# Performance work log

Hardware: AMD Instinct MI355X
Metric: run time of the kernel (lower is better)

## Reference

```python
import jax, jax.numpy as jnp
import numpy as np

B, S, D, H = 256, 512, 128, 256  # batch, seq_len, input_dim, hidden_dim


def setup_inputs() -> dict:
    key = jax.random.key(0)
    ks = jax.random.split(key, 7)
    scale = 1.0 / np.sqrt(H)
    return {
        "x": jax.random.normal(ks[0], (B, S, D), dtype=jnp.float32),
        # WU_e: Linear(2H + S -> S, bias=False)
        "W_ue": jax.random.uniform(ks[1], (S, 2 * H + S), dtype=jnp.float32, minval=-scale, maxval=scale),
        # v_e: Linear(S -> 1, bias=False)
        "v_e": jax.random.uniform(ks[2], (1, S), dtype=jnp.float32, minval=-scale, maxval=scale),
        # LSTM params (PyTorch layout: gates order i,f,g,o)
        "W_ih": jax.random.uniform(ks[3], (4 * H, D), dtype=jnp.float32, minval=-scale, maxval=scale),
        "W_hh": jax.random.uniform(ks[4], (4 * H, H), dtype=jnp.float32, minval=-scale, maxval=scale),
        "b_ih": jax.random.uniform(ks[5], (4 * H,), dtype=jnp.float32, minval=-scale, maxval=scale),
        "b_hh": jax.random.uniform(ks[6], (4 * H,), dtype=jnp.float32, minval=-scale, maxval=scale),
    }


def reference(x, W_ue, v_e, W_ih, W_hh, b_ih, b_hh):
    b = x.shape[0]
    hdim = W_hh.shape[1]
    # Split WU_e into the part acting on (h,c) and the part acting on x rows.
    W_h = W_ue[:, : 2 * hdim]          # [S, 2H]
    W_x = W_ue[:, 2 * hdim:]           # [S, S]
    xT = jnp.transpose(x, (0, 2, 1))   # [B, D, S]
    # x contribution to attention logits is the same every step -> precompute.
    proj_x = jnp.einsum("bds,os->bdo", xT, W_x)  # [B, D, S]
    v = v_e[0]                          # [S]
    xs = jnp.transpose(x, (1, 0, 2))    # [S, B, D]

    def step(carry, x_t):
        h, c = carry                                    # [B, H] each
        hs = jnp.concatenate([h, c], axis=-1)           # [B, 2H]
        proj_h = hs @ W_h.T                             # [B, S]
        t = jnp.tanh(proj_h[:, None, :] + proj_x)       # [B, D, S]
        E = jnp.einsum("bds,s->bd", t, v)               # [B, D]
        alpha = jax.nn.softmax(E, axis=1)               # [B, D]
        inp = x_t * alpha                               # [B, D]
        gates = inp @ W_ih.T + b_ih + h @ W_hh.T + b_hh # [B, 4H]
        i, f, g, o = jnp.split(gates, 4, axis=-1)
        i = jax.nn.sigmoid(i)
        f = jax.nn.sigmoid(f)
        g = jnp.tanh(g)
        o = jax.nn.sigmoid(o)
        c_new = f * c + i * g
        h_new = o * jnp.tanh(c_new)
        return (h_new, c_new), h_new

    h0 = jnp.zeros((b, hdim), dtype=x.dtype)
    c0 = jnp.zeros((b, hdim), dtype=x.dtype)
    _, x_encoded = jax.lax.scan(step, (h0, c0), xs)  # [S, B, H]
    return x_encoded
```

## Files before the change

### kernel.cpp

```cpp
#include <hip/hip_runtime.h>
#include <hip/hip_bf16.h>

typedef __attribute__((ext_vector_type(8))) short bf16x8;
typedef __attribute__((ext_vector_type(4))) float f32x4;

#define C2LE 2.8853900817779268f
#define LOG2E 1.4426950408889634f
#define AGENT __HIP_MEMORY_SCOPE_AGENT
#define RLX __ATOMIC_RELAXED

static __device__ __forceinline__ float blo(unsigned q) { return __uint_as_float(q << 16); }
static __device__ __forceinline__ float bhi(unsigned q) { return __uint_as_float(q & 0xFFFF0000u); }
static __device__ __forceinline__ float sigm(float x) {
  return __builtin_amdgcn_rcpf(1.0f + __builtin_amdgcn_exp2f(-x * LOG2E));
}
static __device__ __forceinline__ float tanhe(float x) {
  return fmaf(-2.0f, __builtin_amdgcn_rcpf(1.0f + __builtin_amdgcn_exp2f(x * C2LE)), 1.0f);
}
static __device__ __forceinline__ unsigned packhilo(float x) {
  __hip_bfloat16 h = __float2bfloat16(x);
  float r = x - __bfloat162float(h);
  __hip_bfloat16 l = __float2bfloat16(r);
  return (unsigned)__bfloat16_as_ushort(h) | ((unsigned)__bfloat16_as_ushort(l) << 16);
}
static __device__ __forceinline__ void mkfrags(uint4 q0, uint4 q1, bf16x8& hi, bf16x8& lo) {
  uint4 h, l;
  h.x = __builtin_amdgcn_perm(q0.y, q0.x, 0x05040100u);
  h.y = __builtin_amdgcn_perm(q0.w, q0.z, 0x05040100u);
  h.z = __builtin_amdgcn_perm(q1.y, q1.x, 0x05040100u);
  h.w = __builtin_amdgcn_perm(q1.w, q1.z, 0x05040100u);
  l.x = __builtin_amdgcn_perm(q0.y, q0.x, 0x07060302u);
  l.y = __builtin_amdgcn_perm(q0.w, q0.z, 0x07060302u);
  l.z = __builtin_amdgcn_perm(q1.y, q1.x, 0x07060302u);
  l.w = __builtin_amdgcn_perm(q1.w, q1.z, 0x07060302u);
  hi = *(bf16x8*)&h;
  lo = *(bf16x8*)&l;
}
static __device__ __forceinline__ int swz(int e) { return e ^ ((e >> 4) & 7); }

__global__ void k_pack_whB(const float* __restrict__ wue, __hip_bfloat16* __restrict__ wp) {
  for (int idx = blockIdx.x * blockDim.x + threadIdx.x; idx < 262144;
       idx += gridDim.x * blockDim.x) {
    int j = idx & 7, l = (idx >> 3) & 63, kap = (idx >> 9) & 15, nb = (idx >> 13) & 3,
        sl = idx >> 15;
    int o = sl * 64 + nb * 16 + (l & 15);
    int dim = kap * 32 + (l >> 4) * 8 + j;
    wp[idx] = __float2bfloat16(wue[o * 1024 + dim]);
  }
}
__global__ void k_pack_w3B(const float* __restrict__ wih, const float* __restrict__ whh,
                           __hip_bfloat16* __restrict__ wp) {
  for (int idx = blockIdx.x * blockDim.x + threadIdx.x; idx < 393216;
       idx += gridDim.x * blockDim.x) {
    int j = idx & 7, l = (idx >> 3) & 63;
    int ks = (idx >> 9) % 12, r = (idx >> 9) / 12;
    int nb = r & 7, sl = r >> 3;
    int n = nb * 16 + (l & 15);
    int g = (n >> 5) * 256 + sl * 32 + (n & 31);
    int k = ks * 32 + (l >> 4) * 8 + j;
    float v = (k < 128) ? wih[g * 128 + k] : whh[g * 256 + (k - 128)];
    wp[idx] = __float2bfloat16(v);
  }
}
__global__ void k_bsum(const float* __restrict__ bih, const float* __restrict__ bhh,
                       float* __restrict__ bs) {
  int idx = blockIdx.x * blockDim.x + threadIdx.x;
  if (idx < 1024) bs[idx] = bih[idx] + bhh[idx];
}
__global__ void k_wxt(const float* __restrict__ wue, float* __restrict__ wxt) {
  for (int idx = blockIdx.x * blockDim.x + threadIdx.x; idx < 512 * 512;
       idx += gridDim.x * blockDim.x) {
    int o = idx & 511, s = idx >> 9;
    wxt[idx] = wue[o * 1024 + 512 + s];
  }
}

__global__ __launch_bounds__(512) void k_projx(const float* __restrict__ x,
                                               const float* __restrict__ wxt,
                                               __hip_bfloat16* __restrict__ px2) {
  __shared__ alignas(16) float xsT[32][512];
  const int b = blockIdx.x;
  const int tid = threadIdx.x;
  for (int dt = 0; dt < 4; ++dt) {
    __syncthreads();
    const float4* xr = (const float4*)(x + ((size_t)b << 16) + (size_t)tid * 128 + dt * 32);
#pragma unroll
    for (int q = 0; q < 8; ++q) {
      float4 vx = xr[q];
      xsT[q * 4 + 0][tid] = vx.x;
      xsT[q * 4 + 1][tid] = vx.y;
      xsT[q * 4 + 2][tid] = vx.z;
      xsT[q * 4 + 3][tid] = vx.w;
    }
    __syncthreads();
    const int o = tid;
    float acc[32];
#pragma unroll
    for (int dd = 0; dd < 32; ++dd) acc[dd] = 0.f;
    for (int s4 = 0; s4 < 128; ++s4) {
      float w0 = wxt[(s4 * 4 + 0) * 512 + o];
      float w1 = wxt[(s4 * 4 + 1) * 512 + o];
      float w2 = wxt[(s4 * 4 + 2) * 512 + o];
      float w3 = wxt[(s4 * 4 + 3) * 512 + o];
#pragma unroll
      for (int dd = 0; dd < 32; ++dd) {
        float4 xv = *(const float4*)&xsT[dd][s4 * 4];
        acc[dd] = fmaf(w0, xv.x, fmaf(w1, xv.y, fmaf(w2, xv.z, fmaf(w3, xv.w, acc[dd]))));
      }
    }
    for (int dd = 0; dd < 32; ++dd) {
      px2[((size_t)b * 128 + dt * 32 + dd) * 512 + o] =
          __float2bfloat16(__builtin_amdgcn_exp2f(acc[dd] * C2LE));
    }
  }
}

__global__ __launch_bounds__(1024) void k_main(
    const __hip_bfloat16* __restrict__ px2, const __hip_bfloat16* __restrict__ whB,
    const __hip_bfloat16* __restrict__ w3B, const float* __restrict__ bsum,
    const float* __restrict__ x, const float* __restrict__ ve,
    unsigned* __restrict__ hG, float* __restrict__ Eg, unsigned* __restrict__ ctrs,
    float* __restrict__ out) {
  __shared__ alignas(16) __hip_bfloat16 w3_l[49152];
  __shared__ alignas(16) uint4 hA0[1024];
  __shared__ alignas(16) uint4 hA1[1024];
  __shared__ alignas(16) uint4 uA0[256];
  __shared__ alignas(16) uint4 uA1[256];
  __shared__ float PHp[4][8][64];
  __shared__ float PH[512];
  __shared__ float gp[2][128][9];
  __shared__ float c_l[32][8];
  __shared__ float v_l[64];
  __shared__ float bs_l[128];
  __shared__ float zpart[16];
  __shared__ float vss_sh;

  const int grp = blockIdx.x & 31;
  const int sl = blockIdx.x >> 5;
  const int tid = threadIdx.x;
  const int lane = tid & 63;
  const int w = tid >> 6;
  const int b = tid >> 7;
  const int d = tid & 127;
  const int bG = grp * 8 + b;

  {
    const uint4* src = (const uint4*)(w3B + (size_t)sl * 49152);
    uint4* dst = (uint4*)w3_l;
    for (int i = tid; i < 6144; i += 1024) dst[i] = src[i];
  }
  bf16x8 whr[4];
  {
    const bf16x8* src =
        (const bf16x8*)whB + ((size_t)(sl * 4 + (w & 3)) * 16 + (w >> 2) * 4) * 64 + lane;
#pragma unroll
    for (int i = 0; i < 4; ++i) whr[i] = src[i * 64];
  }
  uint4 pxr[8];
  {
    const uint4* p4 = (const uint4*)(px2 + ((size_t)bG * 128 + d) * 512 + sl * 64);
#pragma unroll
    for (int i = 0; i < 8; ++i) pxr[i] = p4[i];
  }
  if (tid < 64) v_l[tid] = ve[sl * 64 + tid];
  if (tid < 128) bs_l[tid] = bsum[(tid >> 5) * 256 + sl * 32 + (tid & 31)];
  if (tid < 256) c_l[tid >> 3][tid & 7] = 0.f;
  {
    uint4 z = {0, 0, 0, 0};
    hA0[tid] = z;
    hA1[tid] = z;
    if (tid < 256) {
      uA0[tid] = z;
      uA1[tid] = z;
    }
  }
  if (tid == 0) {
    float s = 0.f;
    for (int i = 0; i < 64; ++i) s += ve[sl * 64 + i];
    vss_sh = s;
  }
  __syncthreads();
  const float vss = vss_sh;
  unsigned* ctrA = ctrs + grp * 64;
  unsigned* ctrB = ctrA + 32;
  float xv = x[((size_t)bG * 512) * 128 + d];

  for (int t = 0; t < 512; ++t) {
    const int par = t & 1;

    {
      const unsigned long long* hp =
          (const unsigned long long*)(hG + (size_t)(par * 32 + grp) * 4096) + tid * 2;
      unsigned long long a0 = __hip_atomic_load(hp, RLX, AGENT);
      unsigned long long a1 = __hip_atomic_load(hp + 1, RLX, AGENT);
      int p = tid * 4;
      int e = ((p >> 6) << 4) + ((p >> 3) & 7);
      int ep = swz(e);
      uint4 q;
      q.x = (unsigned)a0;
      q.y = (unsigned)(a0 >> 32);
      q.z = (unsigned)a1;
      q.w = (unsigned)(a1 >> 32);
      if (p & 4) hA1[ep] = q;
      else hA0[ep] = q;
    }
    if (tid < 128)
      __hip_atomic_store(Eg + (size_t)((1 - par) * 32 + grp) * 1024 + sl * 128 + tid, 0.f, RLX,
                         AGENT);
    __syncthreads();

    {
      const int kq = w >> 2, nb = w & 3;
      f32x4 acc = {0.f, 0.f, 0.f, 0.f};
#pragma unroll
      for (int i = 0; i < 4; ++i) {
        int ep = swz((kq * 4 + i) * 64 + lane);
        uint4 q0 = hA0[ep], q1 = hA1[ep];
        bf16x8 ahi, alo;
        mkfrags(q0, q1, ahi, alo);
        acc = __builtin_amdgcn_mfma_f32_16x16x32_bf16(ahi, whr[i], acc, 0, 0, 0);
        acc = __builtin_amdgcn_mfma_f32_16x16x32_bf16(alo, whr[i], acc, 0, 0, 0);
      }
      if (lane < 32) {
        int r16 = lane >> 4, c16 = lane & 15;
#pragma unroll
        for (int rr = 0; rr < 4; ++rr) PHp[kq][r16 * 4 + rr][nb * 16 + c16] = acc[rr];
      }
    }
    __syncthreads();
    if (tid < 512) {
      float s = (PHp[0][tid >> 6][tid & 63] + PHp[1][tid >> 6][tid & 63] +
                 PHp[2][tid >> 6][tid & 63] + PHp[3][tid >> 6][tid & 63]);
      PH[tid] = __builtin_amdgcn_exp2f(s * C2LE);
    }
    __syncthreads();

    {
      float R = 0.f;
      const float* PHb = &PH[b * 64];
#pragma unroll 2
      for (int s8 = 0; s8 < 8; ++s8) {
        uint4 q = pxr[s8];
        float4 pa = *(const float4*)&PHb[s8 * 8];
        float4 pb = *(const float4*)&PHb[s8 * 8 + 4];
        float4 va = *(const float4*)&v_l[s8 * 8];
        float4 vb = *(const float4*)&v_l[s8 * 8 + 4];
        R = fmaf(va.x, __builtin_amdgcn_rcpf(fmaf(blo(q.x), pa.x, 1.0f)), R);
        R = fmaf(va.y, __builtin_amdgcn_rcpf(fmaf(bhi(q.x), pa.y, 1.0f)), R);
        R = fmaf(va.z, __builtin_amdgcn_rcpf(fmaf(blo(q.y), pa.z, 1.0f)), R);
        R = fmaf(va.w, __builtin_amdgcn_rcpf(fmaf(bhi(q.y), pa.w, 1.0f)), R);
        R = fmaf(vb.x, __builtin_amdgcn_rcpf(fmaf(blo(q.z), pb.x, 1.0f)), R);
        R = fmaf(vb.y, __builtin_amdgcn_rcpf(fmaf(bhi(q.z), pb.y, 1.0f)), R);
        R = fmaf(vb.z, __builtin_amdgcn_rcpf(fmaf(blo(q.w), pb.z, 1.0f)), R);
        R = fmaf(vb.w, __builtin_amdgcn_rcpf(fmaf(bhi(q.w), pb.w, 1.0f)), R);
      }
      __hip_atomic_fetch_add(Eg + (size_t)(par * 32 + grp) * 1024 + b * 128 + d,
                             fmaf(-2.f, R, vss), RLX, AGENT);
    }

    const int nb3 = w & 7, kh3 = w >> 3;
    f32x4 acc3 = {0.f, 0.f, 0.f, 0.f};
#pragma unroll
    for (int i = 0; i < 4; ++i) {
      int ks = 4 + kh3 * 4 + i;
      int ep = swz((ks - 4) * 64 + lane);
      uint4 q0 = hA0[ep], q1 = hA1[ep];
      bf16x8 ahi, alo;
      mkfrags(q0, q1, ahi, alo);
      bf16x8 bf = ((const bf16x8*)w3_l)[((size_t)nb3 * 12 + ks) * 64 + lane];
      acc3 = __builtin_amdgcn_mfma_f32_16x16x32_bf16(ahi, bf, acc3, 0, 0, 0);
      acc3 = __builtin_amdgcn_mfma_f32_16x16x32_bf16(alo, bf, acc3, 0, 0, 0);
    }
    __syncthreads();
    if (tid == 0) {
      __hip_atomic_fetch_add(ctrA, 1u, RLX, AGENT);
      while (__hip_atomic_load(ctrA, RLX, AGENT) < 8u * (t + 1)) __builtin_amdgcn_s_sleep(1);
    }
    __syncthreads();

    float Ev = __hip_atomic_load(Eg + (size_t)(par * 32 + grp) * 1024 + b * 128 + d, RLX, AGENT);
    float e = __builtin_amdgcn_exp2f(Ev * LOG2E);
    {
      float z = e;
#pragma unroll
      for (int m = 1; m < 64; m <<= 1) z += __shfl_xor(z, m);
      if (lane == 0) zpart[w] = z;
    }
    __syncthreads();
    {
      float zf = zpart[2 * b] + zpart[2 * b + 1];
      float u = xv * e * __builtin_amdgcn_rcpf(zf);
      int ep = swz((d >> 5) * 64 + ((d >> 3) & 3) * 16 + b);
      unsigned* dst = (d & 4) ? (unsigned*)&uA1[ep] : (unsigned*)&uA0[ep];
      dst[d & 3] = packhilo(u);
    }
    __syncthreads();

#pragma unroll
    for (int i = 0; i < 2; ++i) {
      int ks = kh3 * 2 + i;
      int ep = swz(ks * 64 + lane);
      uint4 q0 = uA0[ep], q1 = uA1[ep];
      bf16x8 ahi, alo;
      mkfrags(q0, q1, ahi, alo);
      bf16x8 bf = ((const bf16x8*)w3_l)[((size_t)nb3 * 12 + ks) * 64 + lane];
      acc3 = __builtin_amdgcn_mfma_f32_16x16x32_bf16(ahi, bf, acc3, 0, 0, 0);
      acc3 = __builtin_amdgcn_mfma_f32_16x16x32_bf16(alo, bf, acc3, 0, 0, 0);
    }
    if (lane < 32) {
      int r16 = lane >> 4, c16 = lane & 15;
#pragma unroll
      for (int rr = 0; rr < 4; ++rr) gp[kh3][nb3 * 16 + c16][r16 * 4 + rr] = acc3[rr];
    }
    __syncthreads();

    float h_new;
    if (tid < 256) {
      int bb = tid & 7, jj = tid >> 3;
      float gi = gp[0][jj][bb] + gp[1][jj][bb] + bs_l[jj];
      float gf = gp[0][32 + jj][bb] + gp[1][32 + jj][bb] + bs_l[32 + jj];
      float gg = gp[0][64 + jj][bb] + gp[1][64 + jj][bb] + bs_l[64 + jj];
      float go = gp[0][96 + jj][bb] + gp[1][96 + jj][bb] + bs_l[96 + jj];
      float i_ = sigm(gi), f_ = sigm(gf), g_ = tanhe(gg), o_ = sigm(go);
      float c_new = fmaf(f_, c_l[jj][bb], i_ * g_);
      h_new = o_ * tanhe(c_new);
      c_l[jj][bb] = c_new;
      int dd = sl * 32 + jj;
      int p = (((dd >> 5) * 4 + ((dd >> 3) & 3)) * 8 + bb) * 8 + (dd & 7);
      unsigned* hw = hG + (size_t)((1 - par) * 32 + grp) * 4096;
      __hip_atomic_store(hw + p, packhilo(h_new), RLX, AGENT);
      __hip_atomic_store(hw + p + 2048, packhilo(c_new), RLX, AGENT);
    }
    __syncthreads();
    if (tid == 0) __hip_atomic_fetch_add(ctrB, 1u, RLX, AGENT);
    if (tid < 256) {
      int bb = tid & 7, jj = tid >> 3;
      __builtin_nontemporal_store(h_new,
                                  out + ((size_t)t * 256 + grp * 8 + bb) * 256 + sl * 32 + jj);
    }
    int tn = (t < 511) ? t + 1 : 511;
    float xv_n = x[((size_t)bG * 512 + tn) * 128 + d];
    if (tid == 0) {
      while (__hip_atomic_load(ctrB, RLX, AGENT) < 8u * (t + 1)) __builtin_amdgcn_s_sleep(1);
    }
    __syncthreads();
    xv = xv_n;
  }
}

extern "C" void kernel_launch(void* const* d_in, const int* in_sizes, int n_in,
                              void* d_out, int out_size, void* d_ws, size_t ws_size,
                              hipStream_t stream) {
  const float* x = (const float*)d_in[0];
  const float* wue = (const float*)d_in[1];
  const float* ve = (const float*)d_in[2];
  const float* wih = (const float*)d_in[3];
  const float* whh = (const float*)d_in[4];
  const float* bih = (const float*)d_in[5];
  const float* bhh = (const float*)d_in[6];
  float* out = (float*)d_out;

  char* ws = (char*)d_ws;
  __hip_bfloat16* px2 = (__hip_bfloat16*)(ws);
  __hip_bfloat16* whB = (__hip_bfloat16*)(ws + 33554432);
  __hip_bfloat16* w3B = (__hip_bfloat16*)(ws + 34078720);
  float* bsum = (float*)(ws + 34865152);
  float* Eg = (float*)(ws + 34869248);
  unsigned* ctrs = (unsigned*)(ws + 35131392);
  unsigned* hG = (unsigned*)(ws + 35139584);
  float* wxt = (float*)(ws + 36188160);

  k_pack_whB<<<1024, 256, 0, stream>>>(wue, whB);
  k_pack_w3B<<<1024, 256, 0, stream>>>(wih, whh, w3B);
  k_bsum<<<4, 256, 0, stream>>>(bih, bhh, bsum);
  k_wxt<<<256, 256, 0, stream>>>(wue, wxt);
  k_projx<<<256, 512, 0, stream>>>(x, wxt, px2);
  hipMemsetAsync(hG, 0, 1048576, stream);
  hipMemsetAsync(Eg, 0, 262144, stream);
  hipMemsetAsync(ctrs, 0, 8192, stream);
  k_main<<<256, 1024, 0, stream>>>(px2, whB, w3B, bsum, x, ve, hG, Eg, ctrs, out);
}
```

Measured before the change: 4.631 ms.

## Replace atomic-add and counter barrier with step-tagged per-slice E partials

Each of the 8 slice blocks in a group now writes its partial attention logit as a 64-bit word tagged with the step number into its own slot, instead of atomically adding into a shared double-buffered accumulator. Consumers poll all 8 slots until every tag reaches the current step, then sum the partials locally. This removes the float atomic adds, the per-step zeroing of the other buffer, and the tid-0 counter barrier with its two __syncthreads. The cost is 8x more polling loads per thread and a larger buffer. The Eg region now overlaps wxt, which is only read by the earlier k_projx and is zeroed by a memset issued after it.

Result: slower. 8.315 ms (+79.6%).

```diff
diff --git a/kernel.cpp b/kernel.cpp
--- a/kernel.cpp
+++ b/kernel.cpp
@@ -119,8 +119,8 @@
     const __hip_bfloat16* __restrict__ px2, const __hip_bfloat16* __restrict__ whB,
     const __hip_bfloat16* __restrict__ w3B, const float* __restrict__ bsum,
     const float* __restrict__ x, const float* __restrict__ ve,
-    unsigned* __restrict__ hG, float* __restrict__ Eg, unsigned* __restrict__ ctrs,
-    float* __restrict__ out) {
+    unsigned* __restrict__ hG, unsigned long long* __restrict__ Eg,
+    unsigned* __restrict__ ctrs, float* __restrict__ out) {
   __shared__ alignas(16) __hip_bfloat16 w3_l[49152];
   __shared__ alignas(16) uint4 hA0[1024];
   __shared__ alignas(16) uint4 hA1[1024];
@@ -181,8 +181,7 @@
   }
   __syncthreads();
   const float vss = vss_sh;
-  unsigned* ctrA = ctrs + grp * 64;
-  unsigned* ctrB = ctrA + 32;
+  unsigned* ctrB = ctrs + grp * 64 + 32;
   float xv = x[((size_t)bG * 512) * 128 + d];
 
   for (int t = 0; t < 512; ++t) {
@@ -204,9 +203,6 @@
       if (p & 4) hA1[ep] = q;
       else hA0[ep] = q;
     }
-    if (tid < 128)
-      __hip_atomic_store(Eg + (size_t)((1 - par) * 32 + grp) * 1024 + sl * 128 + tid, 0.f, RLX,
-                         AGENT);
     __syncthreads();
 
     {
@@ -254,8 +250,10 @@
         R = fmaf(vb.z, __builtin_amdgcn_rcpf(fmaf(blo(q.w), pb.z, 1.0f)), R);
         R = fmaf(vb.w, __builtin_amdgcn_rcpf(fmaf(bhi(q.w), pb.w, 1.0f)), R);
       }
-      __hip_atomic_fetch_add(Eg + (size_t)(par * 32 + grp) * 1024 + b * 128 + d,
-                             fmaf(-2.f, R, vss), RLX, AGENT);
+      float part = fmaf(-2.f, R, vss);
+      unsigned long long pk =
+          ((unsigned long long)(unsigned)(t + 1) << 32) | (unsigned long long)__float_as_uint(part);
+      __hip_atomic_store(Eg + ((size_t)grp * 8 + sl) * 1024 + b * 128 + d, pk, RLX, AGENT);
     }
 
     const int nb3 = w & 7, kh3 = w >> 3;
@@ -271,15 +269,35 @@
       acc3 = __builtin_amdgcn_mfma_f32_16x16x32_bf16(ahi, bf, acc3, 0, 0, 0);
       acc3 = __builtin_amdgcn_mfma_f32_16x16x32_bf16(alo, bf, acc3, 0, 0, 0);
     }
-    __syncthreads();
-    if (tid == 0) {
-      __hip_atomic_fetch_add(ctrA, 1u, RLX, AGENT);
-      while (__hip_atomic_load(ctrA, RLX, AGENT) < 8u * (t + 1)) __builtin_amdgcn_s_sleep(1);
-    }
-    __syncthreads();
-
-    float Ev = __hip_atomic_load(Eg + (size_t)(par * 32 + grp) * 1024 + b * 128 + d, RLX, AGENT);
-    float e = __builtin_amdgcn_exp2f(Ev * LOG2E);
+
+    float Esum;
+    {
+      const unsigned long long* ep = Eg + (size_t)grp * 8192 + b * 128 + d;
+      const unsigned tgt = (unsigned)(t + 1);
+      unsigned long long v0, v1, v2, v3, v4, v5, v6, v7;
+      for (;;) {
+        v0 = __hip_atomic_load(ep + 0 * 1024, RLX, AGENT);
+        v1 = __hip_atomic_load(ep + 1 * 1024, RLX, AGENT);
+        v2 = __hip_atomic_load(ep + 2 * 1024, RLX, AGENT);
+        v3 = __hip_atomic_load(ep + 3 * 1024, RLX, AGENT);
+        v4 = __hip_atomic_load(ep + 4 * 1024, RLX, AGENT);
+        v5 = __hip_atomic_load(ep + 5 * 1024, RLX, AGENT);
+        v6 = __hip_atomic_load(ep + 6 * 1024, RLX, AGENT);
+        v7 = __hip_atomic_load(ep + 7 * 1024, RLX, AGENT);
+        bool ok = (unsigned)(v0 >> 32) >= tgt && (unsigned)(v1 >> 32) >= tgt &&
+                  (unsigned)(v2 >> 32) >= tgt && (unsigned)(v3 >> 32) >= tgt &&
+                  (unsigned)(v4 >> 32) >= tgt && (unsigned)(v5 >> 32) >= tgt &&
+                  (unsigned)(v6 >> 32) >= tgt && (unsigned)(v7 >> 32) >= tgt;
+        if (__all(ok)) break;
+        __builtin_amdgcn_s_sleep(1);
+      }
+      Esum = ((__uint_as_float((unsigned)v0) + __uint_as_float((unsigned)v1)) +
+              (__uint_as_float((unsigned)v2) + __uint_as_float((unsigned)v3))) +
+             ((__uint_as_float((unsigned)v4) + __uint_as_float((unsigned)v5)) +
+              (__uint_as_float((unsigned)v6) + __uint_as_float((unsigned)v7)));
+    }
+
+    float e = __builtin_amdgcn_exp2f(Esum * LOG2E);
     {
       float z = e;
 #pragma unroll
@@ -365,10 +383,10 @@
   __hip_bfloat16* whB = (__hip_bfloat16*)(ws + 33554432);
   __hip_bfloat16* w3B = (__hip_bfloat16*)(ws + 34078720);
   float* bsum = (float*)(ws + 34865152);
-  float* Eg = (float*)(ws + 34869248);
-  unsigned* ctrs = (unsigned*)(ws + 35131392);
-  unsigned* hG = (unsigned*)(ws + 35139584);
-  float* wxt = (float*)(ws + 36188160);
+  unsigned* ctrs = (unsigned*)(ws + 34869248);
+  unsigned* hG = (unsigned*)(ws + 34877440);
+  unsigned long long* Eg = (unsigned long long*)(ws + 35926016);
+  float* wxt = (float*)(ws + 35926016);
 
   k_pack_whB<<<1024, 256, 0, stream>>>(wue, whB);
   k_pack_w3B<<<1024, 256, 0, stream>>>(wih, whh, w3B);
@@ -376,7 +394,7 @@
   k_wxt<<<256, 256, 0, stream>>>(wue, wxt);
   k_projx<<<256, 512, 0, stream>>>(x, wxt, px2);
   hipMemsetAsync(hG, 0, 1048576, stream);
-  hipMemsetAsync(Eg, 0, 262144, stream);
+  hipMemsetAsync(Eg, 0, 2097152, stream);
   hipMemsetAsync(ctrs, 0, 8192, stream);
   k_main<<<256, 1024, 0, stream>>>(px2, whB, w3B, bsum, x, ve, hG, Eg, ctrs, out);
 }
```

## Split recurrent state into bf16 hi/lo planes and fold softmax into fewer passes

Applied to the files above, without the earlier changes.

Hidden and cell state in global memory and in LDS is now stored as separate high and low bf16 planes. MFMA A-fragments can then be loaded directly instead of being rebuilt with perm instructions every step; writers pair neighbouring lanes with a shuffle to emit the split words. The softmax stage now has 512 threads each handle two elements with a float2 load, which removes the partial-sum array and one block barrier per timestep. Gate-thread indexing is remapped so output stores are more contiguous. The attention logits are now read with a plain load rather than an atomic load, which relies on the counter barrier for visibility.

After: 4.576 ms. Within noise of the previous version (-1.2%).

```diff
diff --git a/kernel.cpp b/kernel.cpp
--- a/kernel.cpp
+++ b/kernel.cpp
@@ -22,19 +22,6 @@
   float r = x - __bfloat162float(h);
   __hip_bfloat16 l = __float2bfloat16(r);
   return (unsigned)__bfloat16_as_ushort(h) | ((unsigned)__bfloat16_as_ushort(l) << 16);
-}
-static __device__ __forceinline__ void mkfrags(uint4 q0, uint4 q1, bf16x8& hi, bf16x8& lo) {
-  uint4 h, l;
-  h.x = __builtin_amdgcn_perm(q0.y, q0.x, 0x05040100u);
-  h.y = __builtin_amdgcn_perm(q0.w, q0.z, 0x05040100u);
-  h.z = __builtin_amdgcn_perm(q1.y, q1.x, 0x05040100u);
-  h.w = __builtin_amdgcn_perm(q1.w, q1.z, 0x05040100u);
-  l.x = __builtin_amdgcn_perm(q0.y, q0.x, 0x07060302u);
-  l.y = __builtin_amdgcn_perm(q0.w, q0.z, 0x07060302u);
-  l.z = __builtin_amdgcn_perm(q1.y, q1.x, 0x07060302u);
-  l.w = __builtin_amdgcn_perm(q1.w, q1.z, 0x07060302u);
-  hi = *(bf16x8*)&h;
-  lo = *(bf16x8*)&l;
 }
 static __device__ __forceinline__ int swz(int e) { return e ^ ((e >> 4) & 7); }
 
@@ -122,17 +109,16 @@
     unsigned* __restrict__ hG, float* __restrict__ Eg, unsigned* __restrict__ ctrs,
     float* __restrict__ out) {
   __shared__ alignas(16) __hip_bfloat16 w3_l[49152];
-  __shared__ alignas(16) uint4 hA0[1024];
-  __shared__ alignas(16) uint4 hA1[1024];
-  __shared__ alignas(16) uint4 uA0[256];
-  __shared__ alignas(16) uint4 uA1[256];
+  __shared__ alignas(16) uint4 hAhi[1024];
+  __shared__ alignas(16) uint4 hAlo[1024];
+  __shared__ alignas(16) uint4 uAhi[256];
+  __shared__ alignas(16) uint4 uAlo[256];
   __shared__ float PHp[4][8][64];
   __shared__ float PH[512];
   __shared__ float gp[2][128][9];
-  __shared__ float c_l[32][8];
+  __shared__ float c_l[32][9];
   __shared__ float v_l[64];
   __shared__ float bs_l[128];
-  __shared__ float zpart[16];
   __shared__ float vss_sh;
 
   const int grp = blockIdx.x & 31;
@@ -140,9 +126,9 @@
   const int tid = threadIdx.x;
   const int lane = tid & 63;
   const int w = tid >> 6;
-  const int b = tid >> 7;
-  const int d = tid & 127;
-  const int bG = grp * 8 + b;
+  const int b2 = tid >> 7;
+  const int d2 = tid & 127;
+  const int bG2 = grp * 8 + b2;
 
   {
     const uint4* src = (const uint4*)(w3B + (size_t)sl * 49152);
@@ -158,7 +144,7 @@
   }
   uint4 pxr[8];
   {
-    const uint4* p4 = (const uint4*)(px2 + ((size_t)bG * 128 + d) * 512 + sl * 64);
+    const uint4* p4 = (const uint4*)(px2 + ((size_t)bG2 * 128 + d2) * 512 + sl * 64);
 #pragma unroll
     for (int i = 0; i < 8; ++i) pxr[i] = p4[i];
   }
@@ -167,11 +153,11 @@
   if (tid < 256) c_l[tid >> 3][tid & 7] = 0.f;
   {
     uint4 z = {0, 0, 0, 0};
-    hA0[tid] = z;
-    hA1[tid] = z;
+    hAhi[tid] = z;
+    hAlo[tid] = z;
     if (tid < 256) {
-      uA0[tid] = z;
-      uA1[tid] = z;
+      uAhi[tid] = z;
+      uAlo[tid] = z;
     }
   }
   if (tid == 0) {
@@ -183,26 +169,28 @@
   const float vss = vss_sh;
   unsigned* ctrA = ctrs + grp * 64;
   unsigned* ctrB = ctrA + 32;
-  float xv = x[((size_t)bG * 512) * 128 + d];
+  float2 xv2;
+  if (tid < 512)
+    xv2 = *(const float2*)&x[((size_t)(grp * 8 + (tid >> 6)) * 512) * 128 + 2 * (tid & 63)];
 
   for (int t = 0; t < 512; ++t) {
     const int par = t & 1;
 
     {
       const unsigned long long* hp =
-          (const unsigned long long*)(hG + (size_t)(par * 32 + grp) * 4096) + tid * 2;
-      unsigned long long a0 = __hip_atomic_load(hp, RLX, AGENT);
-      unsigned long long a1 = __hip_atomic_load(hp + 1, RLX, AGENT);
-      int p = tid * 4;
-      int e = ((p >> 6) << 4) + ((p >> 3) & 7);
-      int ep = swz(e);
+          (const unsigned long long*)(hG + (size_t)(par * 32 + grp) * 4096);
+      int E = tid >> 1, which = tid & 1;
+      const unsigned long long* src = hp + which * 1024 + E * 2;
+      unsigned long long a0 = __hip_atomic_load(src, RLX, AGENT);
+      unsigned long long a1 = __hip_atomic_load(src + 1, RLX, AGENT);
+      int ep = swz(((E >> 3) << 4) + (E & 7));
       uint4 q;
       q.x = (unsigned)a0;
       q.y = (unsigned)(a0 >> 32);
       q.z = (unsigned)a1;
       q.w = (unsigned)(a1 >> 32);
-      if (p & 4) hA1[ep] = q;
-      else hA0[ep] = q;
+      if (which) hAlo[ep] = q;
+      else hAhi[ep] = q;
     }
     if (tid < 128)
       __hip_atomic_store(Eg + (size_t)((1 - par) * 32 + grp) * 1024 + sl * 128 + tid, 0.f, RLX,
@@ -215,9 +203,8 @@
 #pragma unroll
       for (int i = 0; i < 4; ++i) {
         int ep = swz((kq * 4 + i) * 64 + lane);
-        uint4 q0 = hA0[ep], q1 = hA1[ep];
-        bf16x8 ahi, alo;
-        mkfrags(q0, q1, ahi, alo);
+        bf16x8 ahi = *(const bf16x8*)&hAhi[ep];
+        bf16x8 alo = *(const bf16x8*)&hAlo[ep];
         acc = __builtin_amdgcn_mfma_f32_16x16x32_bf16(ahi, whr[i], acc, 0, 0, 0);
         acc = __builtin_amdgcn_mfma_f32_16x16x32_bf16(alo, whr[i], acc, 0, 0, 0);
       }
@@ -237,7 +224,7 @@
 
     {
       float R = 0.f;
-      const float* PHb = &PH[b * 64];
+      const float* PHb = &PH[b2 * 64];
 #pragma unroll 2
       for (int s8 = 0; s8 < 8; ++s8) {
         uint4 q = pxr[s8];
@@ -254,7 +241,7 @@
         R = fmaf(vb.z, __builtin_amdgcn_rcpf(fmaf(blo(q.w), pb.z, 1.0f)), R);
         R = fmaf(vb.w, __builtin_amdgcn_rcpf(fmaf(bhi(q.w), pb.w, 1.0f)), R);
       }
-      __hip_atomic_fetch_add(Eg + (size_t)(par * 32 + grp) * 1024 + b * 128 + d,
+      __hip_atomic_fetch_add(Eg + (size_t)(par * 32 + grp) * 1024 + b2 * 128 + d2,
                              fmaf(-2.f, R, vss), RLX, AGENT);
     }
 
@@ -264,9 +251,8 @@
     for (int i = 0; i < 4; ++i) {
       int ks = 4 + kh3 * 4 + i;
       int ep = swz((ks - 4) * 64 + lane);
-      uint4 q0 = hA0[ep], q1 = hA1[ep];
-      bf16x8 ahi, alo;
-      mkfrags(q0, q1, ahi, alo);
+      bf16x8 ahi = *(const bf16x8*)&hAhi[ep];
+      bf16x8 alo = *(const bf16x8*)&hAlo[ep];
       bf16x8 bf = ((const bf16x8*)w3_l)[((size_t)nb3 * 12 + ks) * 64 + lane];
       acc3 = __builtin_amdgcn_mfma_f32_16x16x32_bf16(ahi, bf, acc3, 0, 0, 0);
       acc3 = __builtin_amdgcn_mfma_f32_16x16x32_bf16(alo, bf, acc3, 0, 0, 0);
@@ -278,21 +264,25 @@
     }
     __syncthreads();
 
-    float Ev = __hip_atomic_load(Eg + (size_t)(par * 32 + grp) * 1024 + b * 128 + d, RLX, AGENT);
-    float e = __builtin_amdgcn_exp2f(Ev * LOG2E);
-    {
-      float z = e;
+    if (tid < 512) {
+      const int bs = tid >> 6, k = tid & 63;
+      float2 Ev = *(const float2*)&((
+          const float*)Eg)[(size_t)(par * 32 + grp) * 1024 + bs * 128 + 2 * k];
+      float e0 = __builtin_amdgcn_exp2f(Ev.x * LOG2E);
+      float e1 = __builtin_amdgcn_exp2f(Ev.y * LOG2E);
+      float z = e0 + e1;
 #pragma unroll
       for (int m = 1; m < 64; m <<= 1) z += __shfl_xor(z, m);
-      if (lane == 0) zpart[w] = z;
-    }
-    __syncthreads();
-    {
-      float zf = zpart[2 * b] + zpart[2 * b + 1];
-      float u = xv * e * __builtin_amdgcn_rcpf(zf);
-      int ep = swz((d >> 5) * 64 + ((d >> 3) & 3) * 16 + b);
-      unsigned* dst = (d & 4) ? (unsigned*)&uA1[ep] : (unsigned*)&uA0[ep];
-      dst[d & 3] = packhilo(u);
+      float zinv = __builtin_amdgcn_rcpf(z);
+      float u0 = xv2.x * e0 * zinv, u1 = xv2.y * e1 * zinv;
+      unsigned pk0 = packhilo(u0), pk1 = packhilo(u1);
+      unsigned whi = __builtin_amdgcn_perm(pk1, pk0, 0x05040100u);
+      unsigned wlo = __builtin_amdgcn_perm(pk1, pk0, 0x07060302u);
+      int d0 = 2 * k;
+      int ep = swz((d0 >> 5) * 64 + ((d0 >> 3) & 3) * 16 + bs);
+      int j2 = (d0 >> 1) & 3;
+      ((unsigned*)&uAhi[ep])[j2] = whi;
+      ((unsigned*)&uAlo[ep])[j2] = wlo;
     }
     __syncthreads();
 
@@ -300,9 +290,8 @@
     for (int i = 0; i < 2; ++i) {
       int ks = kh3 * 2 + i;
       int ep = swz(ks * 64 + lane);
-      uint4 q0 = uA0[ep], q1 = uA1[ep];
-      bf16x8 ahi, alo;
-      mkfrags(q0, q1, ahi, alo);
+      bf16x8 ahi = *(const bf16x8*)&uAhi[ep];
+      bf16x8 alo = *(const bf16x8*)&uAlo[ep];
       bf16x8 bf = ((const bf16x8*)w3_l)[((size_t)nb3 * 12 + ks) * 64 + lane];
       acc3 = __builtin_amdgcn_mfma_f32_16x16x32_bf16(ahi, bf, acc3, 0, 0, 0);
       acc3 = __builtin_amdgcn_mfma_f32_16x16x32_bf16(alo, bf, acc3, 0, 0, 0);
@@ -315,8 +304,8 @@
     __syncthreads();
 
     float h_new;
+    int bb = tid >> 5, jj = tid & 31;
     if (tid < 256) {
-      int bb = tid & 7, jj = tid >> 3;
       float gi = gp[0][jj][bb] + gp[1][jj][bb] + bs_l[jj];
       float gf = gp[0][32 + jj][bb] + gp[1][32 + jj][bb] + bs_l[32 + jj];
       float gg = gp[0][64 + jj][bb] + gp[1][64 + jj][bb] + bs_l[64 + jj];
@@ -325,26 +314,39 @@
       float c_new = fmaf(f_, c_l[jj][bb], i_ * g_);
       h_new = o_ * tanhe(c_new);
       c_l[jj][bb] = c_new;
+      unsigned pkh = packhilo(h_new), pkc = packhilo(c_new);
+      unsigned prh = __shfl_xor(pkh, 1), prc = __shfl_xor(pkc, 1);
       int dd = sl * 32 + jj;
-      int p = (((dd >> 5) * 4 + ((dd >> 3) & 3)) * 8 + bb) * 8 + (dd & 7);
+      int E = ((dd >> 5) * 4 + ((dd >> 3) & 3)) * 8 + bb;
+      int j2 = (dd & 7) >> 1;
       unsigned* hw = hG + (size_t)((1 - par) * 32 + grp) * 4096;
-      __hip_atomic_store(hw + p, packhilo(h_new), RLX, AGENT);
-      __hip_atomic_store(hw + p + 2048, packhilo(c_new), RLX, AGENT);
+      if ((jj & 1) == 0) {
+        __hip_atomic_store(hw + E * 4 + j2, __builtin_amdgcn_perm(prh, pkh, 0x05040100u), RLX,
+                           AGENT);
+        __hip_atomic_store(hw + (E + 256) * 4 + j2, __builtin_amdgcn_perm(prc, pkc, 0x05040100u),
+                           RLX, AGENT);
+      } else {
+        __hip_atomic_store(hw + 2048 + E * 4 + j2, __builtin_amdgcn_perm(pkh, prh, 0x07060302u),
+                           RLX, AGENT);
+        __hip_atomic_store(hw + 2048 + (E + 256) * 4 + j2,
+                           __builtin_amdgcn_perm(pkc, prc, 0x07060302u), RLX, AGENT);
+      }
     }
     __syncthreads();
     if (tid == 0) __hip_atomic_fetch_add(ctrB, 1u, RLX, AGENT);
-    if (tid < 256) {
-      int bb = tid & 7, jj = tid >> 3;
+    if (tid < 256)
       __builtin_nontemporal_store(h_new,
                                   out + ((size_t)t * 256 + grp * 8 + bb) * 256 + sl * 32 + jj);
-    }
-    int tn = (t < 511) ? t + 1 : 511;
-    float xv_n = x[((size_t)bG * 512 + tn) * 128 + d];
+    float2 xv2n;
+    if (tid < 512) {
+      int tn = (t < 511) ? t + 1 : 511;
+      xv2n = *(const float2*)&x[((size_t)(grp * 8 + (tid >> 6)) * 512 + tn) * 128 + 2 * (tid & 63)];
+    }
     if (tid == 0) {
       while (__hip_atomic_load(ctrB, RLX, AGENT) < 8u * (t + 1)) __builtin_amdgcn_s_sleep(1);
     }
     __syncthreads();
-    xv = xv_n;
+    xv2 = xv2n;
   }
 }
 
```
